# Performance work log

Measured on AMD Instinct MI355X. Metric: run time of the kernel, lower is better.

## Reference

```python
import jax, jax.numpy as jnp
import numpy as np

TEMP = 1.0
POOL_K = 0.5
BN_EPS = 1e-5
B, N, D = 16, 256, 128


def setup_inputs() -> dict:
    key = jax.random.key(0)
    ks = jax.random.split(key, 8)
    s = 0.05
    return {
        "x": jax.random.normal(ks[0], (B, N, D), jnp.float32),
        "att_proj_w": jax.random.normal(ks[1], (D, D), jnp.float32) * s,
        "att_proj_b": jnp.zeros((D,), jnp.float32),
        "att_weight": jax.random.normal(ks[2], (D, 1), jnp.float32) * s,
        "pwa_w": jax.random.normal(ks[3], (D, D), jnp.float32) * s,
        "pwa_b": jnp.zeros((D,), jnp.float32),
        "pwoa_w": jax.random.normal(ks[4], (D, D), jnp.float32) * s,
        "pwoa_b": jnp.zeros((D,), jnp.float32),
        "bn_gamma": jnp.ones((D,), jnp.float32),
        "bn_beta": jnp.zeros((D,), jnp.float32),
        "bn_mean": jnp.zeros((D,), jnp.float32),
        "bn_var": jnp.ones((D,), jnp.float32),
        "pool_w": jax.random.normal(ks[5], (D, 1), jnp.float32) * s,
        "pool_b": jnp.zeros((1,), jnp.float32),
    }


def reference(x, att_proj_w, att_proj_b, att_weight, pwa_w, pwa_b,
              pwoa_w, pwoa_b, bn_gamma, bn_beta, bn_mean, bn_var,
              pool_w, pool_b):
    # ---- GraphAttentionLayer (eval mode: dropout = identity) ----
    # pairwise node outer product: (B, N, N, D)
    pair = x[:, :, None, :] * x[:, None, :, :]
    # att_proj + tanh, then project to scalar per node pair
    a = jnp.tanh(pair @ att_proj_w + att_proj_b)          # (B,N,N,D)
    logits = (a @ att_weight)[..., 0] / TEMP              # (B,N,N)
    # softmax over dim=-2 (the first node axis of the (N,N) map)
    att = jax.nn.softmax(logits, axis=1)                  # (B,N,N)
    # project: att_map @ x through proj_with_att, plus skip branch
    agg = jnp.einsum("bij,bjd->bid", att, x)              # (B,N,D)
    h = (agg @ pwa_w + pwa_b) + (x @ pwoa_w + pwoa_b)
    # BatchNorm1d in eval mode over feature dim
    h = (h - bn_mean) * jax.lax.rsqrt(bn_var + BN_EPS) * bn_gamma + bn_beta
    h = jax.nn.selu(h)
    # ---- GraphPool (eval mode: dropout = identity) ----
    scores = jax.nn.sigmoid(h @ pool_w + pool_b)          # (B,N,1)
    k_nodes = max(int(N * POOL_K), 1)
    _, idx = jax.lax.top_k(scores[..., 0], k_nodes)       # (B,k)
    hs = h * scores                                       # (B,N,D)
    out = jnp.take_along_axis(hs, idx[:, :, None], axis=1)  # (B,k,D)
    return out
```

## Files before the change

kernel.cpp:

```cpp
#include <hip/hip_runtime.h>
#include <math.h>

typedef float f32x4 __attribute__((ext_vector_type(4)));
typedef short s16x8 __attribute__((ext_vector_type(8)));

#define L2E 1.4426950408889634f
#define C2L2E 2.885390081777927f

__global__ void k0_prep(const float* __restrict__ W,
                        unsigned short* __restrict__ gWhi,
                        unsigned short* __restrict__ gWlo,
                        float* __restrict__ S) {
  int bid = blockIdx.x;
  if (bid < 64) {
    int t = bid * 256 + threadIdx.x;
    int d = t >> 7, e = t & 127;
    float w = W[d * 128 + e];
    unsigned u = __float_as_uint(w);
    unsigned hb = (u + 0x7fffu + ((u >> 16) & 1u)) >> 16;
    float r = w - __uint_as_float(hb << 16);
    unsigned ul = __float_as_uint(r);
    unsigned lb = (ul + 0x7fffu + ((ul >> 16) & 1u)) >> 16;
    int addr = e * 128 + (d ^ ((e & 7) << 3));
    gWhi[addr] = (unsigned short)hb;
    gWlo[addr] = (unsigned short)lb;
  } else {
    S[(bid - 64) * 256 + threadIdx.x] = 0.f;
  }
}

__global__ __launch_bounds__(256, 2) void kA_logits(
    const float* __restrict__ x, const unsigned short* __restrict__ gWhi,
    const unsigned short* __restrict__ gWlo, const float* __restrict__ apb,
    const float* __restrict__ av, float* __restrict__ Lg,
    float* __restrict__ S) {
  __shared__ __align__(16) unsigned short sWhi[16384];
  __shared__ __align__(16) unsigned short sWlo[16384];
  __shared__ __align__(16) float sXj[16 * 132];
  __shared__ float sRow[16][4];
  __shared__ float sMir[16];

  int tt = blockIdx.x, ti = 0;
  while (tt >= 16 - ti) { tt -= 16 - ti; ++ti; }
  const int tj = ti + tt;
  const int b = blockIdx.y;
  const int i0 = ti * 16, j0 = tj * 16;
  const int tid = threadIdx.x;

  {
    const uint4* shi = (const uint4*)gWhi;
    const uint4* slo = (const uint4*)gWlo;
    uint4* dhi = (uint4*)sWhi;
    uint4* dlo = (uint4*)sWlo;
#pragma unroll
    for (int r = 0; r < 8; ++r) {
      dhi[tid + 256 * r] = shi[tid + 256 * r];
      dlo[tid + 256 * r] = slo[tid + 256 * r];
    }
    const float4* xsrc = (const float4*)(x + ((size_t)(b * 256 + j0)) * 128);
#pragma unroll
    for (int r = 0; r < 2; ++r) {
      int v = tid + 256 * r;
      *(float4*)&sXj[(v >> 5) * 132 + (v & 31) * 4] = xsrc[v];
    }
  }
  __syncthreads();

  const int lane = tid & 63;
  const int w = tid >> 6;
  const int quad = lane >> 4;
  const int col = lane & 15;
  const int swz = (col & 7) << 3;

  float vw[8];
  f32x4 acc[4][8];
#pragma unroll
  for (int et = 0; et < 8; ++et) {
    float bi = apb[col + 16 * et];
    vw[et] = av[col + 16 * et];
#pragma unroll
    for (int mt = 0; mt < 4; ++mt) acc[mt][et] = (f32x4){bi, bi, bi, bi};
  }

  const float* xib = x + ((size_t)(b * 256 + i0 + 4 * w)) * 128;

#pragma unroll
  for (int kstep = 0; kstep < 4; ++kstep) {
    const int k0 = kstep * 32 + quad * 8;
    float4 xj0 = *(const float4*)&sXj[col * 132 + k0];
    float4 xj1 = *(const float4*)&sXj[col * 132 + k0 + 4];
    s16x8 Ah[4], Al[4];
#pragma unroll
    for (int mt = 0; mt < 4; ++mt) {
      const float* xip = xib + mt * 128 + k0;
      float4 xi0 = *(const float4*)xip;
      float4 xi1 = *(const float4*)(xip + 4);
      float pv[8];
      pv[0] = xi0.x * xj0.x; pv[1] = xi0.y * xj0.y;
      pv[2] = xi0.z * xj0.z; pv[3] = xi0.w * xj0.w;
      pv[4] = xi1.x * xj1.x; pv[5] = xi1.y * xj1.y;
      pv[6] = xi1.z * xj1.z; pv[7] = xi1.w * xj1.w;
      uint4 hp, lp;
      unsigned* hq = (unsigned*)&hp;
      unsigned* lq = (unsigned*)&lp;
#pragma unroll
      for (int p = 0; p < 4; ++p) {
        unsigned u0 = __float_as_uint(pv[2 * p]);
        unsigned u1 = __float_as_uint(pv[2 * p + 1]);
        hq[p] = __builtin_amdgcn_perm(u1, u0, 0x07060302);
        float h0 = __uint_as_float(u0 & 0xffff0000u);
        float h1 = __uint_as_float(u1 & 0xffff0000u);
        unsigned v0 = __float_as_uint(pv[2 * p] - h0) + 0x8000u;
        unsigned v1 = __float_as_uint(pv[2 * p + 1] - h1) + 0x8000u;
        lq[p] = __builtin_amdgcn_perm(v1, v0, 0x07060302);
      }
      Ah[mt] = *(s16x8*)&hp;
      Al[mt] = *(s16x8*)&lp;
    }
#pragma unroll
    for (int et = 0; et < 8; ++et) {
      const int addr = (col + 16 * et) * 128 + (k0 ^ swz);
      s16x8 bh = *(const s16x8*)&sWhi[addr];
      s16x8 bl = *(const s16x8*)&sWlo[addr];
#pragma unroll
      for (int mt = 0; mt < 4; ++mt) {
        acc[mt][et] = __builtin_amdgcn_mfma_f32_16x16x32_bf16(Ah[mt], bh, acc[mt][et], 0, 0, 0);
        acc[mt][et] = __builtin_amdgcn_mfma_f32_16x16x32_bf16(Al[mt], bh, acc[mt][et], 0, 0, 0);
        acc[mt][et] = __builtin_amdgcn_mfma_f32_16x16x32_bf16(Ah[mt], bl, acc[mt][et], 0, 0, 0);
      }
    }
  }

  float E[4];
#pragma unroll
  for (int mt = 0; mt < 4; ++mt) {
    float ls[4] = {0.f, 0.f, 0.f, 0.f};
#pragma unroll
    for (int et = 0; et < 8; ++et) {
#pragma unroll
      for (int r = 0; r < 4; ++r) {
        float e2 = __builtin_amdgcn_exp2f(acc[mt][et][r] * C2L2E);
        float t = 1.0f - 2.0f * __builtin_amdgcn_rcpf(e2 + 1.0f);
        ls[r] += t * vw[et];
      }
    }
#pragma unroll
    for (int m = 1; m < 16; m <<= 1) {
      ls[0] += __shfl_xor(ls[0], m);
      ls[1] += __shfl_xor(ls[1], m);
      ls[2] += __shfl_xor(ls[2], m);
      ls[3] += __shfl_xor(ls[3], m);
    }
    float fl = (col == 0) ? ls[0] : (col == 1) ? ls[1] : (col == 2) ? ls[2] : ls[3];
    E[mt] = __builtin_amdgcn_exp2f(fl * L2E);
  }

  if (col < 4) {
    const int j = j0 + quad * 4 + col;
    float4 val = {E[0], E[1], E[2], E[3]};
    *(float4*)&Lg[((size_t)(b * 256 + j)) * 256 + i0 + 4 * w] = val;
    sRow[quad * 4 + col][w] = E[0] + E[1] + E[2] + E[3];
  }

  if (ti != tj) {
    if (col < 4) {
      const int j = j0 + quad * 4 + col;
#pragma unroll
      for (int mt = 0; mt < 4; ++mt)
        Lg[((size_t)(b * 256 + i0 + 4 * w + mt)) * 256 + j] = E[mt];
    }
#pragma unroll
    for (int mt = 0; mt < 4; ++mt) {
      float v = (col < 4) ? E[mt] : 0.f;
#pragma unroll
      for (int m = 1; m < 64; m <<= 1) v += __shfl_xor(v, m);
      if (lane == 0) sMir[4 * w + mt] = v;
    }
  }
  __syncthreads();
  if (tid < 16) {
    atomicAdd(&S[b * 256 + j0 + tid],
              sRow[tid][0] + sRow[tid][1] + sRow[tid][2] + sRow[tid][3]);
    if (ti != tj) atomicAdd(&S[b * 256 + i0 + tid], sMir[tid]);
  }
}

__global__ void kB_aggh(const float* __restrict__ Lg, const float* __restrict__ S,
                        const float* __restrict__ x,
                        const float* __restrict__ pwa, const float* __restrict__ pwoa,
                        const float* __restrict__ pwab, const float* __restrict__ pwob,
                        const float* __restrict__ gam, const float* __restrict__ bet,
                        const float* __restrict__ mea, const float* __restrict__ varr,
                        const float* __restrict__ plw, const float* __restrict__ plb,
                        float* __restrict__ h, float* __restrict__ scores) {
  const int b = blockIdx.y, i0 = blockIdx.x * 8;
  const int tid = threadIdx.x;
  const int il = tid >> 5, dl = tid & 31;
  __shared__ float sInv[256];
  __shared__ float satt[16][8];
  __shared__ float sxj[2048];
  __shared__ float sa[1024];
  __shared__ float sxi[1024];
  __shared__ double sScD[8][32];

  sInv[tid] = 1.0f / S[b * 256 + tid];
  ((float4*)sxi)[tid] = ((const float4*)(x + ((size_t)(b * 256 + i0)) * 128))[tid];

  float acc[4] = {0.f, 0.f, 0.f, 0.f};
  for (int jj = 0; jj < 256; jj += 16) {
    __syncthreads();
    if (tid < 128)
      satt[tid >> 3][tid & 7] =
          Lg[((size_t)(b * 256 + jj + (tid >> 3))) * 256 + i0 + (tid & 7)] *
          sInv[jj + (tid >> 3)];
    const float4* xsrc = (const float4*)(x + ((size_t)(b * 256 + jj)) * 128);
    ((float4*)sxj)[tid] = xsrc[tid];
    ((float4*)sxj)[tid + 256] = xsrc[tid + 256];
    __syncthreads();
#pragma unroll
    for (int jl = 0; jl < 16; ++jl) {
      float a = satt[jl][il];
      float4 xv = *(const float4*)&sxj[jl * 128 + dl * 4];
      acc[0] += a * xv.x; acc[1] += a * xv.y;
      acc[2] += a * xv.z; acc[3] += a * xv.w;
    }
  }
  __syncthreads();
  *(float4*)&sa[il * 128 + dl * 4] = *(float4*)acc;
  __syncthreads();

  double z[4] = {0, 0, 0, 0};
  for (int k = 0; k < 128; ++k) {
    double a = (double)sa[il * 128 + k];
    float4 wv = *(const float4*)(pwa + k * 128 + dl * 4);
    z[0] += a * (double)wv.x; z[1] += a * (double)wv.y;
    z[2] += a * (double)wv.z; z[3] += a * (double)wv.w;
  }
  for (int k = 0; k < 128; ++k) {
    double a = (double)sxi[il * 128 + k];
    float4 wv = *(const float4*)(pwoa + k * 128 + dl * 4);
    z[0] += a * (double)wv.x; z[1] += a * (double)wv.y;
    z[2] += a * (double)wv.z; z[3] += a * (double)wv.w;
  }
  float o[4];
#pragma unroll
  for (int q = 0; q < 4; ++q) {
    int d = dl * 4 + q;
    double hv = z[q] + (double)pwab[d] + (double)pwob[d];
    double bn = (hv - (double)mea[d]) * (1.0 / sqrt((double)varr[d] + 1e-5)) *
                    (double)gam[d] +
                (double)bet[d];
    float bf = (float)bn;
    o[q] = bf > 0.f ? 1.0507009873554805f * bf
                    : 1.7580993408473766f *
                          (__builtin_amdgcn_exp2f(bf * L2E) - 1.0f);
  }
  *(float4*)(h + ((size_t)(b * 256 + i0 + il)) * 128 + dl * 4) = *(float4*)o;

  sScD[il][dl] = (double)o[0] * (double)plw[dl * 4] +
                 (double)o[1] * (double)plw[dl * 4 + 1] +
                 (double)o[2] * (double)plw[dl * 4 + 2] +
                 (double)o[3] * (double)plw[dl * 4 + 3];
  __syncthreads();
  if (tid < 8) {
    double zz = (double)plb[0];
    for (int c = 0; c < 32; ++c) zz += sScD[tid][c];
    scores[b * 256 + i0 + tid] = (float)(1.0 / (1.0 + exp(-zz)));
  }
}

__global__ __launch_bounds__(1024) void kC_topk(const float* __restrict__ h,
                                                const float* __restrict__ scores,
                                                float* __restrict__ out) {
  const int b = blockIdx.x, tid = threadIdx.x;
  const int t = tid >> 2, c = tid & 3;
  __shared__ float sc[256];
  __shared__ int ipart[256][4];
  __shared__ int sel[128];

  if (c == 0) sc[t] = scores[b * 256 + t];
  __syncthreads();
  {
    const float st = sc[t];
    int r = 0;
    for (int m = c * 64; m < c * 64 + 64; ++m) {
      float sm = sc[m];
      r += (sm > st) || (sm == st && m < t);
    }
    ipart[t][c] = r;
  }
  __syncthreads();
  if (c == 0) {
    int rank = ipart[t][0] + ipart[t][1] + ipart[t][2] + ipart[t][3];
    if (rank < 128) sel[rank] = t;
  }
  __syncthreads();
  const float4* h4 = (const float4*)(h + (size_t)b * 256 * 128);
  float4* o4 = (float4*)(out + (size_t)b * 128 * 128);
#pragma unroll
  for (int r = 0; r < 4; ++r) {
    int v = tid + 1024 * r;
    int row = v >> 5, q = v & 31;
    int src = sel[row];
    float ss = sc[src];
    float4 hv = h4[src * 32 + q];
    float4 ov;
    ov.x = hv.x * ss; ov.y = hv.y * ss; ov.z = hv.z * ss; ov.w = hv.w * ss;
    o4[row * 32 + q] = ov;
  }
}

extern "C" void kernel_launch(void* const* d_in, const int* in_sizes, int n_in,
                              void* d_out, int out_size, void* d_ws, size_t ws_size,
                              hipStream_t stream) {
  const float* x    = (const float*)d_in[0];
  const float* apw  = (const float*)d_in[1];
  const float* apb  = (const float*)d_in[2];
  const float* av   = (const float*)d_in[3];
  const float* pwa  = (const float*)d_in[4];
  const float* pwab = (const float*)d_in[5];
  const float* pwoa = (const float*)d_in[6];
  const float* pwob = (const float*)d_in[7];
  const float* gam  = (const float*)d_in[8];
  const float* bet  = (const float*)d_in[9];
  const float* mea  = (const float*)d_in[10];
  const float* varr = (const float*)d_in[11];
  const float* plw  = (const float*)d_in[12];
  const float* plb  = (const float*)d_in[13];
  float* out = (float*)d_out;

  unsigned short* gWhi = (unsigned short*)d_ws;
  unsigned short* gWlo = gWhi + 16384;
  float* S  = (float*)((char*)d_ws + 65536);
  float* Lg = (float*)((char*)d_ws + 81920);
  float* hb = Lg + (size_t)16 * 256 * 256;
  float* sco = hb + (size_t)16 * 256 * 128;

  k0_prep<<<80, 256, 0, stream>>>(apw, gWhi, gWlo, S);
  kA_logits<<<dim3(136, 16), 256, 0, stream>>>(x, gWhi, gWlo, apb, av, Lg, S);
  kB_aggh<<<dim3(32, 16), 256, 0, stream>>>(Lg, S, x, pwa, pwoa, pwab, pwob,
                                            gam, bet, mea, varr, plw, plb, hb, sco);
  kC_topk<<<16, 1024, 0, stream>>>(hb, sco, out);
}
```

Measured before the change: 185.1 us.

## Halve LDS and accumulators in logits kernel, stream low-bf16 weights from global

The logits kernel now keeps only the high bf16 half of the projection weights in shared memory. The low half is pre-arranged by the prep kernel in MFMA fragment order and read straight from global/L2, which halves LDS use. The four-row M tile is split into two passes of two rows, cutting accumulator registers, and launch bounds are raised to three blocks per CU to increase occupancy. The activation hi/lo bf16 split now uses round-to-nearest packing, and the aggregation kernel reads attention rows contiguously with a padded shared tile. The risks are extra global-memory traffic for the weight fragments and the x/sXj reloads repeated in each pass.

```diff
diff --git a/kernel.cpp b/kernel.cpp
--- a/kernel.cpp
+++ b/kernel.cpp
@@ -1,4 +1,5 @@
 #include <hip/hip_runtime.h>
+#include <hip/hip_bf16.h>
 #include <math.h>
 
 typedef float f32x4 __attribute__((ext_vector_type(4)));
@@ -7,9 +8,16 @@
 #define L2E 1.4426950408889634f
 #define C2L2E 2.885390081777927f
 
+__device__ __forceinline__ unsigned pack_bf16x2_rne(float a, float b) {
+  __hip_bfloat162 t = __float22bfloat162_rn(float2{a, b});
+  unsigned r;
+  __builtin_memcpy(&r, &t, 4);
+  return r;
+}
+
 __global__ void k0_prep(const float* __restrict__ W,
                         unsigned short* __restrict__ gWhi,
-                        unsigned short* __restrict__ gWlo,
+                        unsigned short* __restrict__ gBlo,
                         float* __restrict__ S) {
   int bid = blockIdx.x;
   if (bid < 64) {
@@ -18,24 +26,30 @@
     float w = W[d * 128 + e];
     unsigned u = __float_as_uint(w);
     unsigned hb = (u + 0x7fffu + ((u >> 16) & 1u)) >> 16;
+    gWhi[e * 128 + (d ^ ((e & 7) << 3))] = (unsigned short)hb;
+  } else if (bid < 128) {
+    int t = (bid - 64) * 256 + threadIdx.x;
+    int q = t & 7, lane = (t >> 3) & 63, fs = t >> 9;
+    int kstep = fs & 3, et = fs >> 2;
+    int e = (lane & 15) + 16 * et;
+    int k = 32 * kstep + 8 * (lane >> 4) + q;
+    float w = W[k * 128 + e];
+    unsigned u = __float_as_uint(w);
+    unsigned hb = (u + 0x7fffu + ((u >> 16) & 1u)) >> 16;
     float r = w - __uint_as_float(hb << 16);
     unsigned ul = __float_as_uint(r);
-    unsigned lb = (ul + 0x7fffu + ((ul >> 16) & 1u)) >> 16;
-    int addr = e * 128 + (d ^ ((e & 7) << 3));
-    gWhi[addr] = (unsigned short)hb;
-    gWlo[addr] = (unsigned short)lb;
+    gBlo[t] = (unsigned short)((ul + 0x7fffu + ((ul >> 16) & 1u)) >> 16);
   } else {
-    S[(bid - 64) * 256 + threadIdx.x] = 0.f;
-  }
-}
-
-__global__ __launch_bounds__(256, 2) void kA_logits(
+    S[(bid - 128) * 256 + threadIdx.x] = 0.f;
+  }
+}
+
+__global__ __launch_bounds__(256, 3) void kA_logits(
     const float* __restrict__ x, const unsigned short* __restrict__ gWhi,
-    const unsigned short* __restrict__ gWlo, const float* __restrict__ apb,
+    const unsigned short* __restrict__ gBlo, const float* __restrict__ apb,
     const float* __restrict__ av, float* __restrict__ Lg,
     float* __restrict__ S) {
   __shared__ __align__(16) unsigned short sWhi[16384];
-  __shared__ __align__(16) unsigned short sWlo[16384];
   __shared__ __align__(16) float sXj[16 * 132];
   __shared__ float sRow[16][4];
   __shared__ float sMir[16];
@@ -49,14 +63,9 @@
 
   {
     const uint4* shi = (const uint4*)gWhi;
-    const uint4* slo = (const uint4*)gWlo;
     uint4* dhi = (uint4*)sWhi;
-    uint4* dlo = (uint4*)sWlo;
-#pragma unroll
-    for (int r = 0; r < 8; ++r) {
-      dhi[tid + 256 * r] = shi[tid + 256 * r];
-      dlo[tid + 256 * r] = slo[tid + 256 * r];
-    }
+#pragma unroll
+    for (int r = 0; r < 8; ++r) dhi[tid + 256 * r] = shi[tid + 256 * r];
     const float4* xsrc = (const float4*)(x + ((size_t)(b * 256 + j0)) * 128);
 #pragma unroll
     for (int r = 0; r < 2; ++r) {
@@ -72,109 +81,112 @@
   const int col = lane & 15;
   const int swz = (col & 7) << 3;
 
-  float vw[8];
-  f32x4 acc[4][8];
+  float bias[8], vw[8];
 #pragma unroll
   for (int et = 0; et < 8; ++et) {
-    float bi = apb[col + 16 * et];
+    bias[et] = apb[col + 16 * et];
     vw[et] = av[col + 16 * et];
-#pragma unroll
-    for (int mt = 0; mt < 4; ++mt) acc[mt][et] = (f32x4){bi, bi, bi, bi};
   }
 
   const float* xib = x + ((size_t)(b * 256 + i0 + 4 * w)) * 128;
-
-#pragma unroll
-  for (int kstep = 0; kstep < 4; ++kstep) {
-    const int k0 = kstep * 32 + quad * 8;
-    float4 xj0 = *(const float4*)&sXj[col * 132 + k0];
-    float4 xj1 = *(const float4*)&sXj[col * 132 + k0 + 4];
-    s16x8 Ah[4], Al[4];
-#pragma unroll
-    for (int mt = 0; mt < 4; ++mt) {
-      const float* xip = xib + mt * 128 + k0;
-      float4 xi0 = *(const float4*)xip;
-      float4 xi1 = *(const float4*)(xip + 4);
-      float pv[8];
-      pv[0] = xi0.x * xj0.x; pv[1] = xi0.y * xj0.y;
-      pv[2] = xi0.z * xj0.z; pv[3] = xi0.w * xj0.w;
-      pv[4] = xi1.x * xj1.x; pv[5] = xi1.y * xj1.y;
-      pv[6] = xi1.z * xj1.z; pv[7] = xi1.w * xj1.w;
-      uint4 hp, lp;
-      unsigned* hq = (unsigned*)&hp;
-      unsigned* lq = (unsigned*)&lp;
-#pragma unroll
-      for (int p = 0; p < 4; ++p) {
-        unsigned u0 = __float_as_uint(pv[2 * p]);
-        unsigned u1 = __float_as_uint(pv[2 * p + 1]);
-        hq[p] = __builtin_amdgcn_perm(u1, u0, 0x07060302);
-        float h0 = __uint_as_float(u0 & 0xffff0000u);
-        float h1 = __uint_as_float(u1 & 0xffff0000u);
-        unsigned v0 = __float_as_uint(pv[2 * p] - h0) + 0x8000u;
-        unsigned v1 = __float_as_uint(pv[2 * p + 1] - h1) + 0x8000u;
-        lq[p] = __builtin_amdgcn_perm(v1, v0, 0x07060302);
-      }
-      Ah[mt] = *(s16x8*)&hp;
-      Al[mt] = *(s16x8*)&lp;
-    }
+  const unsigned short* gBlL = gBlo + lane * 8;
+
+  for (int p = 0; p < 2; ++p) {
+    f32x4 acc[2][8];
 #pragma unroll
     for (int et = 0; et < 8; ++et) {
-      const int addr = (col + 16 * et) * 128 + (k0 ^ swz);
-      s16x8 bh = *(const s16x8*)&sWhi[addr];
-      s16x8 bl = *(const s16x8*)&sWlo[addr];
-#pragma unroll
-      for (int mt = 0; mt < 4; ++mt) {
-        acc[mt][et] = __builtin_amdgcn_mfma_f32_16x16x32_bf16(Ah[mt], bh, acc[mt][et], 0, 0, 0);
-        acc[mt][et] = __builtin_amdgcn_mfma_f32_16x16x32_bf16(Al[mt], bh, acc[mt][et], 0, 0, 0);
-        acc[mt][et] = __builtin_amdgcn_mfma_f32_16x16x32_bf16(Ah[mt], bl, acc[mt][et], 0, 0, 0);
-      }
-    }
-  }
-
-  float E[4];
-#pragma unroll
-  for (int mt = 0; mt < 4; ++mt) {
-    float ls[4] = {0.f, 0.f, 0.f, 0.f};
-#pragma unroll
-    for (int et = 0; et < 8; ++et) {
-#pragma unroll
-      for (int r = 0; r < 4; ++r) {
-        float e2 = __builtin_amdgcn_exp2f(acc[mt][et][r] * C2L2E);
-        float t = 1.0f - 2.0f * __builtin_amdgcn_rcpf(e2 + 1.0f);
-        ls[r] += t * vw[et];
-      }
-    }
-#pragma unroll
-    for (int m = 1; m < 16; m <<= 1) {
-      ls[0] += __shfl_xor(ls[0], m);
-      ls[1] += __shfl_xor(ls[1], m);
-      ls[2] += __shfl_xor(ls[2], m);
-      ls[3] += __shfl_xor(ls[3], m);
-    }
-    float fl = (col == 0) ? ls[0] : (col == 1) ? ls[1] : (col == 2) ? ls[2] : ls[3];
-    E[mt] = __builtin_amdgcn_exp2f(fl * L2E);
-  }
-
-  if (col < 4) {
-    const int j = j0 + quad * 4 + col;
-    float4 val = {E[0], E[1], E[2], E[3]};
-    *(float4*)&Lg[((size_t)(b * 256 + j)) * 256 + i0 + 4 * w] = val;
-    sRow[quad * 4 + col][w] = E[0] + E[1] + E[2] + E[3];
-  }
-
-  if (ti != tj) {
+      acc[0][et] = (f32x4){bias[et], bias[et], bias[et], bias[et]};
+      acc[1][et] = (f32x4){bias[et], bias[et], bias[et], bias[et]};
+    }
+
+#pragma unroll
+    for (int kstep = 0; kstep < 4; ++kstep) {
+      const int k0 = kstep * 32 + quad * 8;
+      float4 xj0 = *(const float4*)&sXj[col * 132 + k0];
+      float4 xj1 = *(const float4*)&sXj[col * 132 + k0 + 4];
+      s16x8 Ah[2], Al[2];
+#pragma unroll
+      for (int mt = 0; mt < 2; ++mt) {
+        const float* xip = xib + (2 * p + mt) * 128 + k0;
+        float4 xi0 = *(const float4*)xip;
+        float4 xi1 = *(const float4*)(xip + 4);
+        float pv[8];
+        pv[0] = xi0.x * xj0.x; pv[1] = xi0.y * xj0.y;
+        pv[2] = xi0.z * xj0.z; pv[3] = xi0.w * xj0.w;
+        pv[4] = xi1.x * xj1.x; pv[5] = xi1.y * xj1.y;
+        pv[6] = xi1.z * xj1.z; pv[7] = xi1.w * xj1.w;
+        uint4 hp, lp;
+        unsigned* hq = (unsigned*)&hp;
+        unsigned* lq = (unsigned*)&lp;
+#pragma unroll
+        for (int pp = 0; pp < 4; ++pp) {
+          float a = pv[2 * pp], c = pv[2 * pp + 1];
+          unsigned hv = pack_bf16x2_rne(a, c);
+          float h0 = __uint_as_float(hv << 16);
+          float h1 = __uint_as_float(hv & 0xffff0000u);
+          lq[pp] = pack_bf16x2_rne(a - h0, c - h1);
+          hq[pp] = hv;
+        }
+        Ah[mt] = *(s16x8*)&hp;
+        Al[mt] = *(s16x8*)&lp;
+      }
+#pragma unroll
+      for (int et = 0; et < 8; ++et) {
+        s16x8 bh = *(const s16x8*)&sWhi[(col + 16 * et) * 128 + (k0 ^ swz)];
+        s16x8 bl = *(const s16x8*)(gBlL + (et * 4 + kstep) * 512);
+#pragma unroll
+        for (int mt = 0; mt < 2; ++mt) {
+          acc[mt][et] = __builtin_amdgcn_mfma_f32_16x16x32_bf16(Ah[mt], bh, acc[mt][et], 0, 0, 0);
+          acc[mt][et] = __builtin_amdgcn_mfma_f32_16x16x32_bf16(Al[mt], bh, acc[mt][et], 0, 0, 0);
+          acc[mt][et] = __builtin_amdgcn_mfma_f32_16x16x32_bf16(Ah[mt], bl, acc[mt][et], 0, 0, 0);
+        }
+      }
+    }
+
+    float E[2];
+#pragma unroll
+    for (int mt = 0; mt < 2; ++mt) {
+      float ls[4] = {0.f, 0.f, 0.f, 0.f};
+#pragma unroll
+      for (int et = 0; et < 8; ++et) {
+#pragma unroll
+        for (int r = 0; r < 4; ++r) {
+          float e2 = __builtin_amdgcn_exp2f(acc[mt][et][r] * C2L2E);
+          float t = 1.0f - 2.0f * __builtin_amdgcn_rcpf(e2 + 1.0f);
+          ls[r] += t * vw[et];
+        }
+      }
+#pragma unroll
+      for (int m = 1; m < 16; m <<= 1) {
+        ls[0] += __shfl_xor(ls[0], m);
+        ls[1] += __shfl_xor(ls[1], m);
+        ls[2] += __shfl_xor(ls[2], m);
+        ls[3] += __shfl_xor(ls[3], m);
+      }
+      float fl = (col == 0) ? ls[0] : (col == 1) ? ls[1] : (col == 2) ? ls[2] : ls[3];
+      E[mt] = __builtin_amdgcn_exp2f(fl * L2E);
+    }
+
     if (col < 4) {
       const int j = j0 + quad * 4 + col;
-#pragma unroll
-      for (int mt = 0; mt < 4; ++mt)
-        Lg[((size_t)(b * 256 + i0 + 4 * w + mt)) * 256 + j] = E[mt];
-    }
-#pragma unroll
-    for (int mt = 0; mt < 4; ++mt) {
-      float v = (col < 4) ? E[mt] : 0.f;
-#pragma unroll
-      for (int m = 1; m < 64; m <<= 1) v += __shfl_xor(v, m);
-      if (lane == 0) sMir[4 * w + mt] = v;
+      float2 val = {E[0], E[1]};
+      *(float2*)&Lg[((size_t)(b * 256 + j)) * 256 + i0 + 4 * w + 2 * p] = val;
+      float rs = E[0] + E[1];
+      if (p == 0) sRow[quad * 4 + col][w] = rs;
+      else sRow[quad * 4 + col][w] += rs;
+      if (ti != tj) {
+        Lg[((size_t)(b * 256 + i0 + 4 * w + 2 * p)) * 256 + j] = E[0];
+        Lg[((size_t)(b * 256 + i0 + 4 * w + 2 * p + 1)) * 256 + j] = E[1];
+      }
+    }
+    if (ti != tj) {
+#pragma unroll
+      for (int mt = 0; mt < 2; ++mt) {
+        float v = (col < 4) ? E[mt] : 0.f;
+#pragma unroll
+        for (int m = 1; m < 64; m <<= 1) v += __shfl_xor(v, m);
+        if (lane == 0) sMir[4 * w + 2 * p + mt] = v;
+      }
     }
   }
   __syncthreads();
@@ -197,7 +209,7 @@
   const int tid = threadIdx.x;
   const int il = tid >> 5, dl = tid & 31;
   __shared__ float sInv[256];
-  __shared__ float satt[16][8];
+  __shared__ float satt[16][9];
   __shared__ float sxj[2048];
   __shared__ float sa[1024];
   __shared__ float sxi[1024];
@@ -209,10 +221,11 @@
   float acc[4] = {0.f, 0.f, 0.f, 0.f};
   for (int jj = 0; jj < 256; jj += 16) {
     __syncthreads();
-    if (tid < 128)
-      satt[tid >> 3][tid & 7] =
-          Lg[((size_t)(b * 256 + jj + (tid >> 3))) * 256 + i0 + (tid & 7)] *
-          sInv[jj + (tid >> 3)];
+    if (tid < 128) {
+      int ir = tid >> 4, jc = tid & 15;
+      satt[jc][ir] = Lg[((size_t)(b * 256 + i0 + ir)) * 256 + jj + jc] *
+                     sInv[jj + jc];
+    }
     const float4* xsrc = (const float4*)(x + ((size_t)(b * 256 + jj)) * 128);
     ((float4*)sxj)[tid] = xsrc[tid];
     ((float4*)sxj)[tid + 256] = xsrc[tid + 256];
@@ -330,14 +343,14 @@
   float* out = (float*)d_out;
 
   unsigned short* gWhi = (unsigned short*)d_ws;
-  unsigned short* gWlo = gWhi + 16384;
+  unsigned short* gBlo = gWhi + 16384;
   float* S  = (float*)((char*)d_ws + 65536);
   float* Lg = (float*)((char*)d_ws + 81920);
   float* hb = Lg + (size_t)16 * 256 * 256;
   float* sco = hb + (size_t)16 * 256 * 128;
 
-  k0_prep<<<80, 256, 0, stream>>>(apw, gWhi, gWlo, S);
-  kA_logits<<<dim3(136, 16), 256, 0, stream>>>(x, gWhi, gWlo, apb, av, Lg, S);
+  k0_prep<<<144, 256, 0, stream>>>(apw, gWhi, gBlo, S);
+  kA_logits<<<dim3(136, 16), 256, 0, stream>>>(x, gWhi, gBlo, apb, av, Lg, S);
   kB_aggh<<<dim3(32, 16), 256, 0, stream>>>(Lg, S, x, pwa, pwoa, pwab, pwob,
                                             gam, bet, mea, varr, plw, plb, hb, sco);
   kC_topk<<<16, 1024, 0, stream>>>(hb, sco, out);
```

After: 638.8 us. 245% more time.

## Fuse top-k into aggregation kernel and replace atomic column sums with partials

Applied to the files above, without the earlier changes.

Removes the separate top-k kernel launch: the last block to finish each batch (tracked with an atomic counter) performs ranking and gathers the selected rows. Column sums of the exponentials are now written as per-tile partials and reduced in the aggregation kernel, so the zero-init pass and float atomics go away and the sums become deterministic. The aggregation kernel also reads attention rows contiguously from the mirrored logit buffer. In exchange, the top-k tail runs on only one block per batch with 256 threads, and correctness depends on the counter being reset each launch.

```diff
diff --git a/kernel.cpp b/kernel.cpp
--- a/kernel.cpp
+++ b/kernel.cpp
@@ -10,30 +10,26 @@
 __global__ void k0_prep(const float* __restrict__ W,
                         unsigned short* __restrict__ gWhi,
                         unsigned short* __restrict__ gWlo,
-                        float* __restrict__ S) {
-  int bid = blockIdx.x;
-  if (bid < 64) {
-    int t = bid * 256 + threadIdx.x;
-    int d = t >> 7, e = t & 127;
-    float w = W[d * 128 + e];
-    unsigned u = __float_as_uint(w);
-    unsigned hb = (u + 0x7fffu + ((u >> 16) & 1u)) >> 16;
-    float r = w - __uint_as_float(hb << 16);
-    unsigned ul = __float_as_uint(r);
-    unsigned lb = (ul + 0x7fffu + ((ul >> 16) & 1u)) >> 16;
-    int addr = e * 128 + (d ^ ((e & 7) << 3));
-    gWhi[addr] = (unsigned short)hb;
-    gWlo[addr] = (unsigned short)lb;
-  } else {
-    S[(bid - 64) * 256 + threadIdx.x] = 0.f;
-  }
+                        int* __restrict__ cnt) {
+  if (blockIdx.x == 0 && threadIdx.x < 16) cnt[threadIdx.x] = 0;
+  int t = blockIdx.x * 256 + threadIdx.x;
+  int d = t >> 7, e = t & 127;
+  float w = W[d * 128 + e];
+  unsigned u = __float_as_uint(w);
+  unsigned hb = (u + 0x7fffu + ((u >> 16) & 1u)) >> 16;
+  float r = w - __uint_as_float(hb << 16);
+  unsigned ul = __float_as_uint(r);
+  unsigned lb = (ul + 0x7fffu + ((ul >> 16) & 1u)) >> 16;
+  int addr = e * 128 + (d ^ ((e & 7) << 3));
+  gWhi[addr] = (unsigned short)hb;
+  gWlo[addr] = (unsigned short)lb;
 }
 
 __global__ __launch_bounds__(256, 2) void kA_logits(
     const float* __restrict__ x, const unsigned short* __restrict__ gWhi,
     const unsigned short* __restrict__ gWlo, const float* __restrict__ apb,
     const float* __restrict__ av, float* __restrict__ Lg,
-    float* __restrict__ S) {
+    float* __restrict__ Sp) {
   __shared__ __align__(16) unsigned short sWhi[16384];
   __shared__ __align__(16) unsigned short sWlo[16384];
   __shared__ __align__(16) float sXj[16 * 132];
@@ -160,15 +156,13 @@
     float4 val = {E[0], E[1], E[2], E[3]};
     *(float4*)&Lg[((size_t)(b * 256 + j)) * 256 + i0 + 4 * w] = val;
     sRow[quad * 4 + col][w] = E[0] + E[1] + E[2] + E[3];
-  }
-
-  if (ti != tj) {
-    if (col < 4) {
-      const int j = j0 + quad * 4 + col;
+    if (ti != tj) {
 #pragma unroll
       for (int mt = 0; mt < 4; ++mt)
         Lg[((size_t)(b * 256 + i0 + 4 * w + mt)) * 256 + j] = E[mt];
     }
+  }
+  if (ti != tj) {
 #pragma unroll
     for (int mt = 0; mt < 4; ++mt) {
       float v = (col < 4) ? E[mt] : 0.f;
@@ -179,41 +173,52 @@
   }
   __syncthreads();
   if (tid < 16) {
-    atomicAdd(&S[b * 256 + j0 + tid],
-              sRow[tid][0] + sRow[tid][1] + sRow[tid][2] + sRow[tid][3]);
-    if (ti != tj) atomicAdd(&S[b * 256 + i0 + tid], sMir[tid]);
+    Sp[((size_t)(b * 256 + j0 + tid)) * 16 + ti] =
+        sRow[tid][0] + sRow[tid][1] + sRow[tid][2] + sRow[tid][3];
+    if (ti != tj) Sp[((size_t)(b * 256 + i0 + tid)) * 16 + tj] = sMir[tid];
   }
 }
 
-__global__ void kB_aggh(const float* __restrict__ Lg, const float* __restrict__ S,
+__global__ void kB_aggh(const float* __restrict__ Lg, const float* __restrict__ Sp,
                         const float* __restrict__ x,
                         const float* __restrict__ pwa, const float* __restrict__ pwoa,
                         const float* __restrict__ pwab, const float* __restrict__ pwob,
                         const float* __restrict__ gam, const float* __restrict__ bet,
                         const float* __restrict__ mea, const float* __restrict__ varr,
                         const float* __restrict__ plw, const float* __restrict__ plb,
-                        float* __restrict__ h, float* __restrict__ scores) {
-  const int b = blockIdx.y, i0 = blockIdx.x * 8;
+                        float* __restrict__ h, float* __restrict__ scores,
+                        int* __restrict__ cnt, float* __restrict__ out) {
+  const int bb = blockIdx.y, i0 = blockIdx.x * 8;
   const int tid = threadIdx.x;
   const int il = tid >> 5, dl = tid & 31;
   __shared__ float sInv[256];
-  __shared__ float satt[16][8];
+  __shared__ float satt[16][9];
   __shared__ float sxj[2048];
   __shared__ float sa[1024];
   __shared__ float sxi[1024];
   __shared__ double sScD[8][32];
-
-  sInv[tid] = 1.0f / S[b * 256 + tid];
-  ((float4*)sxi)[tid] = ((const float4*)(x + ((size_t)(b * 256 + i0)) * 128))[tid];
+  __shared__ int sLast;
+  __shared__ float sc[256];
+  __shared__ int sel[128];
+
+  {
+    const float4* sp = (const float4*)(Sp + ((size_t)(bb * 256 + tid)) * 16);
+    float4 p0 = sp[0], p1 = sp[1], p2 = sp[2], p3 = sp[3];
+    float s = ((p0.x + p0.y) + (p0.z + p0.w)) + ((p1.x + p1.y) + (p1.z + p1.w)) +
+              ((p2.x + p2.y) + (p2.z + p2.w)) + ((p3.x + p3.y) + (p3.z + p3.w));
+    sInv[tid] = 1.0f / s;
+  }
+  ((float4*)sxi)[tid] = ((const float4*)(x + ((size_t)(bb * 256 + i0)) * 128))[tid];
 
   float acc[4] = {0.f, 0.f, 0.f, 0.f};
   for (int jj = 0; jj < 256; jj += 16) {
     __syncthreads();
-    if (tid < 128)
-      satt[tid >> 3][tid & 7] =
-          Lg[((size_t)(b * 256 + jj + (tid >> 3))) * 256 + i0 + (tid & 7)] *
-          sInv[jj + (tid >> 3)];
-    const float4* xsrc = (const float4*)(x + ((size_t)(b * 256 + jj)) * 128);
+    if (tid < 128) {
+      int ir = tid >> 4, jc = tid & 15;
+      satt[jc][ir] = Lg[((size_t)(bb * 256 + i0 + ir)) * 256 + jj + jc] *
+                     sInv[jj + jc];
+    }
+    const float4* xsrc = (const float4*)(x + ((size_t)(bb * 256 + jj)) * 128);
     ((float4*)sxj)[tid] = xsrc[tid];
     ((float4*)sxj)[tid + 256] = xsrc[tid + 256];
     __syncthreads();
@@ -255,7 +260,7 @@
                     : 1.7580993408473766f *
                           (__builtin_amdgcn_exp2f(bf * L2E) - 1.0f);
   }
-  *(float4*)(h + ((size_t)(b * 256 + i0 + il)) * 128 + dl * 4) = *(float4*)o;
+  *(float4*)(h + ((size_t)(bb * 256 + i0 + il)) * 128 + dl * 4) = *(float4*)o;
 
   sScD[il][dl] = (double)o[0] * (double)plw[dl * 4] +
                  (double)o[1] * (double)plw[dl * 4 + 1] +
@@ -265,41 +270,33 @@
   if (tid < 8) {
     double zz = (double)plb[0];
     for (int c = 0; c < 32; ++c) zz += sScD[tid][c];
-    scores[b * 256 + i0 + tid] = (float)(1.0 / (1.0 + exp(-zz)));
-  }
-}
-
-__global__ __launch_bounds__(1024) void kC_topk(const float* __restrict__ h,
-                                                const float* __restrict__ scores,
-                                                float* __restrict__ out) {
-  const int b = blockIdx.x, tid = threadIdx.x;
-  const int t = tid >> 2, c = tid & 3;
-  __shared__ float sc[256];
-  __shared__ int ipart[256][4];
-  __shared__ int sel[128];
-
-  if (c == 0) sc[t] = scores[b * 256 + t];
+    scores[bb * 256 + i0 + tid] = (float)(1.0 / (1.0 + exp(-zz)));
+  }
+
+  __threadfence();
+  __syncthreads();
+  if (tid == 0) sLast = (atomicAdd(&cnt[bb], 1) == 31);
+  __syncthreads();
+  if (!sLast) return;
+  __threadfence();
+
+  sc[tid] = scores[bb * 256 + tid];
   __syncthreads();
   {
-    const float st = sc[t];
+    const float st = sc[tid];
     int r = 0;
-    for (int m = c * 64; m < c * 64 + 64; ++m) {
+    for (int m = 0; m < 256; ++m) {
       float sm = sc[m];
-      r += (sm > st) || (sm == st && m < t);
-    }
-    ipart[t][c] = r;
-  }
-  __syncthreads();
-  if (c == 0) {
-    int rank = ipart[t][0] + ipart[t][1] + ipart[t][2] + ipart[t][3];
-    if (rank < 128) sel[rank] = t;
-  }
-  __syncthreads();
-  const float4* h4 = (const float4*)(h + (size_t)b * 256 * 128);
-  float4* o4 = (float4*)(out + (size_t)b * 128 * 128);
-#pragma unroll
-  for (int r = 0; r < 4; ++r) {
-    int v = tid + 1024 * r;
+      r += (sm > st) || (sm == st && m < tid);
+    }
+    if (r < 128) sel[r] = tid;
+  }
+  __syncthreads();
+  const float4* h4 = (const float4*)(h + (size_t)bb * 256 * 128);
+  float4* o4 = (float4*)(out + (size_t)bb * 128 * 128);
+#pragma unroll
+  for (int rr = 0; rr < 16; ++rr) {
+    int v = tid + 256 * rr;
     int row = v >> 5, q = v & 31;
     int src = sel[row];
     float ss = sc[src];
@@ -331,14 +328,15 @@
 
   unsigned short* gWhi = (unsigned short*)d_ws;
   unsigned short* gWlo = gWhi + 16384;
-  float* S  = (float*)((char*)d_ws + 65536);
-  float* Lg = (float*)((char*)d_ws + 81920);
-  float* hb = Lg + (size_t)16 * 256 * 256;
+  int*   cnt = (int*)((char*)d_ws + 65536);
+  float* Sp  = (float*)((char*)d_ws + 66560);
+  float* Lg  = (float*)((char*)d_ws + 66560 + 262144);
+  float* hb  = Lg + (size_t)16 * 256 * 256;
   float* sco = hb + (size_t)16 * 256 * 128;
 
-  k0_prep<<<80, 256, 0, stream>>>(apw, gWhi, gWlo, S);
-  kA_logits<<<dim3(136, 16), 256, 0, stream>>>(x, gWhi, gWlo, apb, av, Lg, S);
-  kB_aggh<<<dim3(32, 16), 256, 0, stream>>>(Lg, S, x, pwa, pwoa, pwab, pwob,
-                                            gam, bet, mea, varr, plw, plb, hb, sco);
-  kC_topk<<<16, 1024, 0, stream>>>(hb, sco, out);
+  k0_prep<<<64, 256, 0, stream>>>(apw, gWhi, gWlo, cnt);
+  kA_logits<<<dim3(136, 16), 256, 0, stream>>>(x, gWhi, gWlo, apb, av, Lg, Sp);
+  kB_aggh<<<dim3(32, 16), 256, 0, stream>>>(Lg, Sp, x, pwa, pwoa, pwab, pwob,
+                                            gam, bet, mea, varr, plw, plb, hb,
+                                            sco, cnt, out);
 }
```

Measured after the change: 225.6 us. 21.8% more time.
